# Kernel tuning notes

Measured on AMD Instinct MI355X. Metric: run time of the kernel, lower is better.

The kernel has to match this reference:

```python
import jax, jax.numpy as jnp
import numpy as np

NUM_QUBITS = 4
NUM_LAYERS = 1
CHANNELS = 12
CNOT_CHAIN = [(0, 1), (1, 2), (2, 3), (3, 0)]


def _rz(theta):
    # theta: [B] -> [B,2,2] diag(e^{-i t/2}, e^{i t/2})
    em = jnp.exp(-0.5j * theta)
    ep = jnp.exp(0.5j * theta)
    z = jnp.zeros_like(em)
    return jnp.stack([jnp.stack([em, z], -1), jnp.stack([z, ep], -1)], -2)


def _ry(theta):
    # theta: [B] -> [B,2,2] real rotation, cast to complex
    c = jnp.cos(0.5 * theta)
    s = jnp.sin(0.5 * theta)
    m = jnp.stack([jnp.stack([c, -s], -1), jnp.stack([s, c], -1)], -2)
    return m.astype(jnp.complex64)


def _u3(theta, phi, lam):
    # scalar params -> [2,2] PennyLane U3 convention
    c = jnp.cos(0.5 * theta).astype(jnp.complex64)
    s = jnp.sin(0.5 * theta).astype(jnp.complex64)
    return jnp.stack([
        jnp.stack([c, -jnp.exp(1j * lam) * s]),
        jnp.stack([jnp.exp(1j * phi) * s, jnp.exp(1j * (phi + lam)) * c]),
    ])


def _apply_1q(state, U, wire):
    # state: [B,2,2,2,2]; U: [B,2,2] (batched) or [2,2] (shared)
    state = jnp.moveaxis(state, wire + 1, -1)
    if U.ndim == 3:
        state = jnp.einsum('bij,b...j->b...i', U, state)
    else:
        state = jnp.einsum('ij,b...j->b...i', U, state)
    return jnp.moveaxis(state, -1, wire + 1)


def _cnot(state, ctrl, tgt):
    ax_c, ax_t = ctrl + 1, tgt + 1
    s0 = jnp.take(state, 0, axis=ax_c)
    s1 = jnp.take(state, 1, axis=ax_c)
    t_ax = ax_t if ax_t < ax_c else ax_t - 1  # target axis after removing ctrl axis
    s1 = jnp.flip(s1, axis=t_ax)
    return jnp.stack([s0, s1], axis=ax_c)


def _vqc(enc_angles, weights):
    # enc_angles: [B,4,3] float32; weights: [L,4,3] float32 -> [B,4] Z-expectations
    B = enc_angles.shape[0]
    # H on all qubits from |0000> gives uniform real amplitudes 1/4
    state = jnp.full((B,) + (2,) * NUM_QUBITS, 0.25, dtype=jnp.complex64)
    for w in range(NUM_QUBITS):
        state = _apply_1q(state, _rz(enc_angles[:, w, 0]), w)
        state = _apply_1q(state, _ry(enc_angles[:, w, 1]), w)
        state = _apply_1q(state, _rz(enc_angles[:, w, 2]), w)
    for l in range(weights.shape[0]):
        for c, t in CNOT_CHAIN:
            state = _cnot(state, c, t)
        for w in range(NUM_QUBITS):
            state = _apply_1q(state, _u3(weights[l, w, 0], weights[l, w, 1], weights[l, w, 2]), w)
    probs = jnp.real(state * jnp.conj(state))  # [B,2,2,2,2]
    zs = []
    for w in range(NUM_QUBITS):
        p = jnp.moveaxis(probs, w + 1, 1).reshape(B, 2, -1).sum(-1)
        zs.append(p[:, 0] - p[:, 1])
    return jnp.stack(zs, axis=1)


def setup_inputs() -> dict:
    key = jax.random.key(0)
    kx, kw, kfw, kfb = jax.random.split(key, 4)
    B, C, H, W = 64, CHANNELS, 256, 256
    x = jax.random.normal(kx, (B, C, H, W), dtype=jnp.float32)
    vqc_weights = jax.random.normal(kw, (NUM_LAYERS, NUM_QUBITS, 3), dtype=jnp.float32)
    bound = 1.0 / np.sqrt(NUM_QUBITS)
    fc_w = jax.random.uniform(kfw, (CHANNELS, NUM_QUBITS), jnp.float32, -bound, bound)
    fc_b = jax.random.uniform(kfb, (CHANNELS,), jnp.float32, -bound, bound)
    return {"x": x, "vqc_weights": vqc_weights, "fc_w": fc_w, "fc_b": fc_b}


def reference(x, vqc_weights, fc_w, fc_b):
    B, C, H, W = x.shape
    y = x.mean(axis=(2, 3))                    # AdaptiveAvgPool2d(1) -> [B,C]
    enc_angles = y.reshape(B, NUM_QUBITS, 3)
    q_out = _vqc(enc_angles, vqc_weights)      # [B,4]
    att = jax.nn.sigmoid(q_out @ fc_w.T + fc_b)  # [B,C]
    return x * att[:, :, None, None]
```

## Files before the change

### kernel.cpp

```cpp
#include <hip/hip_runtime.h>
#include <math.h>

#define HW 65536
#define HW4 16384
#define NPLANES 768
#define NQ 4
#define NCH 12

__global__ __launch_bounds__(512) void mean_kernel(const float* __restrict__ x,
                                                   float* __restrict__ y) {
    const int plane = blockIdx.x;
    const float4* p = reinterpret_cast<const float4*>(x) + (size_t)plane * HW4;
    float sum = 0.f;
    for (int i = threadIdx.x; i < HW4; i += blockDim.x) {
        float4 v = p[i];
        sum += (v.x + v.y) + (v.z + v.w);
    }
    #pragma unroll
    for (int off = 32; off > 0; off >>= 1) sum += __shfl_down(sum, off);
    __shared__ float wsum[8];
    const int lane = threadIdx.x & 63;
    const int wid  = threadIdx.x >> 6;
    if (lane == 0) wsum[wid] = sum;
    __syncthreads();
    if (threadIdx.x == 0) {
        float t = 0.f;
        #pragma unroll
        for (int i = 0; i < 8; ++i) t += wsum[i];
        y[plane] = t * (1.0f / (float)HW);
    }
}

__device__ __forceinline__ void apply_rz(float* sr, float* si, int mask, float theta) {
    float c, s;
    __sincosf(0.5f * theta, &s, &c);
    #pragma unroll
    for (int i = 0; i < 16; ++i) {
        float r = sr[i], im = si[i];
        if (i & mask) {
            sr[i] = r * c - im * s;
            si[i] = im * c + r * s;
        } else {
            sr[i] = r * c + im * s;
            si[i] = im * c - r * s;
        }
    }
}

__device__ __forceinline__ void apply_ry(float* sr, float* si, int mask, float theta) {
    float c, s;
    __sincosf(0.5f * theta, &s, &c);
    #pragma unroll
    for (int i = 0; i < 16; ++i) {
        if (i & mask) continue;
        int j = i | mask;
        float r0 = sr[i], i0 = si[i], r1 = sr[j], i1 = si[j];
        sr[i] = c * r0 - s * r1;  si[i] = c * i0 - s * i1;
        sr[j] = s * r0 + c * r1;  si[j] = s * i0 + c * i1;
    }
}

__device__ __forceinline__ void apply_cnot(float* sr, float* si, int mc, int mt) {
    #pragma unroll
    for (int i = 0; i < 16; ++i) {
        if ((i & mc) && !(i & mt)) {
            int j = i | mt;
            float tr = sr[i], ti = si[i];
            sr[i] = sr[j]; si[i] = si[j];
            sr[j] = tr;    si[j] = ti;
        }
    }
}

__device__ __forceinline__ void apply_u3(float* sr, float* si, int mask,
                                         float theta, float phi, float lam) {
    float c = __cosf(0.5f * theta), s = __sinf(0.5f * theta);
    float cl, sl, cp, sp, cpl, spl;
    __sincosf(lam, &sl, &cl);
    __sincosf(phi, &sp, &cp);
    __sincosf(phi + lam, &spl, &cpl);
    float u01r = -cl * s, u01i = -sl * s;
    float u10r =  cp * s, u10i =  sp * s;
    float u11r =  cpl * c, u11i = spl * c;
    #pragma unroll
    for (int i = 0; i < 16; ++i) {
        if (i & mask) continue;
        int j = i | mask;
        float r0 = sr[i], i0 = si[i], r1 = sr[j], i1 = si[j];
        sr[i] = c * r0 + (u01r * r1 - u01i * i1);
        si[i] = c * i0 + (u01r * i1 + u01i * r1);
        sr[j] = (u10r * r0 - u10i * i0) + (u11r * r1 - u11i * i1);
        si[j] = (u10r * i0 + u10i * r0) + (u11r * i1 + u11i * r1);
    }
}

__global__ __launch_bounds__(64) void vqc_kernel(const float* __restrict__ y,
                                                 const float* __restrict__ w,
                                                 const float* __restrict__ fcw,
                                                 const float* __restrict__ fcb,
                                                 float* __restrict__ att) {
    const int b = threadIdx.x;
    float sr[16], si[16];
    #pragma unroll
    for (int i = 0; i < 16; ++i) { sr[i] = 0.25f; si[i] = 0.f; }

    #pragma unroll
    for (int q = 0; q < NQ; ++q) {
        const int mask = 1 << (3 - q);
        float t0 = y[b * NCH + q * 3 + 0];
        float t1 = y[b * NCH + q * 3 + 1];
        float t2 = y[b * NCH + q * 3 + 2];
        apply_rz(sr, si, mask, t0);
        apply_ry(sr, si, mask, t1);
        apply_rz(sr, si, mask, t2);
    }

    apply_cnot(sr, si, 1 << 3, 1 << 2);
    apply_cnot(sr, si, 1 << 2, 1 << 1);
    apply_cnot(sr, si, 1 << 1, 1 << 0);
    apply_cnot(sr, si, 1 << 0, 1 << 3);
    #pragma unroll
    for (int q = 0; q < NQ; ++q) {
        const int mask = 1 << (3 - q);
        apply_u3(sr, si, mask, w[q * 3 + 0], w[q * 3 + 1], w[q * 3 + 2]);
    }

    float z[NQ];
    #pragma unroll
    for (int q = 0; q < NQ; ++q) {
        const int mask = 1 << (3 - q);
        float acc = 0.f;
        #pragma unroll
        for (int i = 0; i < 16; ++i) {
            float p = sr[i] * sr[i] + si[i] * si[i];
            acc += (i & mask) ? -p : p;
        }
        z[q] = acc;
    }

    #pragma unroll
    for (int ch = 0; ch < NCH; ++ch) {
        float a = fcb[ch];
        #pragma unroll
        for (int q = 0; q < NQ; ++q) a += z[q] * fcw[ch * NQ + q];
        att[b * NCH + ch] = 1.0f / (1.0f + expf(-a));
    }
}

__global__ __launch_bounds__(256) void scale_kernel(const float* __restrict__ x,
                                                    const float* __restrict__ att,
                                                    float* __restrict__ out,
                                                    long n4) {
    long i = (long)blockIdx.x * blockDim.x + threadIdx.x;
    const long stride = (long)gridDim.x * blockDim.x;
    const float4* xi = reinterpret_cast<const float4*>(x);
    float4* oi = reinterpret_cast<float4*>(out);
    for (; i < n4; i += stride) {
        float a = att[i >> 14];
        float4 v = xi[i];
        v.x *= a; v.y *= a; v.z *= a; v.w *= a;
        oi[i] = v;
    }
}

extern "C" void kernel_launch(void* const* d_in, const int* in_sizes, int n_in,
                              void* d_out, int out_size, void* d_ws, size_t ws_size,
                              hipStream_t stream) {
    const float* x     = (const float*)d_in[0];
    const float* vqc_w = (const float*)d_in[1];
    const float* fcw   = (const float*)d_in[2];
    const float* fcb   = (const float*)d_in[3];
    float* out = (float*)d_out;

    float* y   = (float*)d_ws;
    float* att = y + NPLANES;

    mean_kernel<<<NPLANES, 512, 0, stream>>>(x, y);
    vqc_kernel<<<1, 64, 0, stream>>>(y, vqc_w, fcw, fcb, att);
    scale_kernel<<<2048, 256, 0, stream>>>(x, att, out, (long)(NPLANES) * HW4);
}
```

Before: 109.8 us.

## Split mean reduction into segment partials, unroll loads, use nontemporal stores in scale

The per-plane mean is now computed by 3072 blocks of 256 threads, each summing a quarter plane with four independent unrolled float4 loads, rather than 768 blocks looping over a whole plane. The VQC kernel finishes the reduction by combining the four partials per plane. The scale kernel unrolls its grid-stride loop and writes the output with nontemporal stores, intended to keep output writes from displacing cached input. The goal is more memory parallelism across the 201 MB of reads, in exchange for an extra small partial buffer.

```diff
diff --git a/kernel.cpp b/kernel.cpp
--- a/kernel.cpp
+++ b/kernel.cpp
@@ -4,31 +4,37 @@
 #define HW 65536
 #define HW4 16384
 #define NPLANES 768
+#define NSEG 3072
+#define SEG4 4096
 #define NQ 4
 #define NCH 12
 
-__global__ __launch_bounds__(512) void mean_kernel(const float* __restrict__ x,
-                                                   float* __restrict__ y) {
-    const int plane = blockIdx.x;
-    const float4* p = reinterpret_cast<const float4*>(x) + (size_t)plane * HW4;
-    float sum = 0.f;
-    for (int i = threadIdx.x; i < HW4; i += blockDim.x) {
-        float4 v = p[i];
-        sum += (v.x + v.y) + (v.z + v.w);
+typedef float f32x4 __attribute__((ext_vector_type(4)));
+
+__global__ __launch_bounds__(256) void mean_partial(const float* __restrict__ x,
+                                                    float* __restrict__ part) {
+    const int seg = blockIdx.x;
+    const f32x4* p = reinterpret_cast<const f32x4*>(x) + (size_t)seg * SEG4;
+    const int t = threadIdx.x;
+    float s0 = 0.f, s1 = 0.f, s2 = 0.f, s3 = 0.f;
+    #pragma unroll
+    for (int i = 0; i < 16; i += 4) {
+        f32x4 a = p[t + (i + 0) * 256];
+        f32x4 b = p[t + (i + 1) * 256];
+        f32x4 c = p[t + (i + 2) * 256];
+        f32x4 d = p[t + (i + 3) * 256];
+        s0 += (a.x + a.y) + (a.z + a.w);
+        s1 += (b.x + b.y) + (b.z + b.w);
+        s2 += (c.x + c.y) + (c.z + c.w);
+        s3 += (d.x + d.y) + (d.z + d.w);
     }
+    float sum = (s0 + s1) + (s2 + s3);
     #pragma unroll
     for (int off = 32; off > 0; off >>= 1) sum += __shfl_down(sum, off);
-    __shared__ float wsum[8];
-    const int lane = threadIdx.x & 63;
-    const int wid  = threadIdx.x >> 6;
-    if (lane == 0) wsum[wid] = sum;
+    __shared__ float wsum[4];
+    if ((threadIdx.x & 63) == 0) wsum[threadIdx.x >> 6] = sum;
     __syncthreads();
-    if (threadIdx.x == 0) {
-        float t = 0.f;
-        #pragma unroll
-        for (int i = 0; i < 8; ++i) t += wsum[i];
-        y[plane] = t * (1.0f / (float)HW);
-    }
+    if (threadIdx.x == 0) part[seg] = (wsum[0] + wsum[1]) + (wsum[2] + wsum[3]);
 }
 
 __device__ __forceinline__ void apply_rz(float* sr, float* si, int mask, float theta) {
@@ -94,12 +100,20 @@
     }
 }
 
-__global__ __launch_bounds__(64) void vqc_kernel(const float* __restrict__ y,
+__global__ __launch_bounds__(64) void vqc_kernel(const float* __restrict__ part,
                                                  const float* __restrict__ w,
                                                  const float* __restrict__ fcw,
                                                  const float* __restrict__ fcb,
                                                  float* __restrict__ att) {
     const int b = threadIdx.x;
+    const f32x4* pp = reinterpret_cast<const f32x4*>(part);
+    float yv[NCH];
+    #pragma unroll
+    for (int c = 0; c < NCH; ++c) {
+        f32x4 v = pp[b * NCH + c];
+        yv[c] = ((v.x + v.y) + (v.z + v.w)) * (1.0f / (float)HW);
+    }
+
     float sr[16], si[16];
     #pragma unroll
     for (int i = 0; i < 16; ++i) { sr[i] = 0.25f; si[i] = 0.f; }
@@ -107,12 +121,9 @@
     #pragma unroll
     for (int q = 0; q < NQ; ++q) {
         const int mask = 1 << (3 - q);
-        float t0 = y[b * NCH + q * 3 + 0];
-        float t1 = y[b * NCH + q * 3 + 1];
-        float t2 = y[b * NCH + q * 3 + 2];
-        apply_rz(sr, si, mask, t0);
-        apply_ry(sr, si, mask, t1);
-        apply_rz(sr, si, mask, t2);
+        apply_rz(sr, si, mask, yv[q * 3 + 0]);
+        apply_ry(sr, si, mask, yv[q * 3 + 1]);
+        apply_rz(sr, si, mask, yv[q * 3 + 2]);
     }
 
     apply_cnot(sr, si, 1 << 3, 1 << 2);
@@ -153,13 +164,14 @@
                                                     long n4) {
     long i = (long)blockIdx.x * blockDim.x + threadIdx.x;
     const long stride = (long)gridDim.x * blockDim.x;
-    const float4* xi = reinterpret_cast<const float4*>(x);
-    float4* oi = reinterpret_cast<float4*>(out);
+    const f32x4* xi = reinterpret_cast<const f32x4*>(x);
+    f32x4* oi = reinterpret_cast<f32x4*>(out);
+    #pragma unroll 4
     for (; i < n4; i += stride) {
         float a = att[i >> 14];
-        float4 v = xi[i];
-        v.x *= a; v.y *= a; v.z *= a; v.w *= a;
-        oi[i] = v;
+        f32x4 v = xi[i];
+        v *= a;
+        __builtin_nontemporal_store(v, &oi[i]);
     }
 }
 
@@ -172,10 +184,10 @@
     const float* fcb   = (const float*)d_in[3];
     float* out = (float*)d_out;
 
-    float* y   = (float*)d_ws;
-    float* att = y + NPLANES;
+    float* part = (float*)d_ws;
+    float* att  = part + NSEG;
 
-    mean_kernel<<<NPLANES, 512, 0, stream>>>(x, y);
-    vqc_kernel<<<1, 64, 0, stream>>>(y, vqc_w, fcw, fcb, att);
-    scale_kernel<<<2048, 256, 0, stream>>>(x, att, out, (long)(NPLANES) * HW4);
+    mean_partial<<<NSEG, 256, 0, stream>>>(x, part);
+    vqc_kernel<<<1, 64, 0, stream>>>(part, vqc_w, fcw, fcb, att);
+    scale_kernel<<<2048, 256, 0, stream>>>(x, att, out, (long)NPLANES * HW4);
 }
```

Result: faster. 100.0 us (-8.9%).
